# Performance work log

Hardware: AMD Instinct MI355X
Metric: run time of the kernel (lower is better)

## Reference

```python
import jax, jax.numpy as jnp
import numpy as np
from jax import lax

IMG_W, IMG_H = 800.0, 320.0
NPTS = 72
N_STRIPS = NPTS - 1
MAX_LANES = 4
NUM_PRIORS = 192
STAGES = 3
B = 512
LIOU_LEN = 15.0
CLS_W, XYT_W, IOU_W, SEG_W = 2.0, 0.2, 2.0, 1.0


def smooth_l1(x):
    ax = jnp.abs(x)
    return jnp.where(ax < 1.0, 0.5 * x * x, ax - 0.5)


def pairwise_line_iou(pred_xs, tgt_xs):
    # pred_xs [P,N] pixel xs, tgt_xs [L,N]; returns [P,L]
    px1, px2 = pred_xs - LIOU_LEN, pred_xs + LIOU_LEN
    tx1, tx2 = tgt_xs - LIOU_LEN, tgt_xs + LIOU_LEN
    ovr = jnp.minimum(px2[:, None, :], tx2[None]) - jnp.maximum(px1[:, None, :], tx1[None])
    union = jnp.maximum(px2[:, None, :], tx2[None]) - jnp.minimum(px1[:, None, :], tx1[None])
    invalid = (tgt_xs < 0) | (tgt_xs >= IMG_W)
    ovr = jnp.where(invalid[None], 0.0, ovr)
    union = jnp.where(invalid[None], 0.0, union)
    return ovr.sum(-1) / (union.sum(-1) + 1e-9)


def focal_sum(logits, target):
    # kornia-style softmax focal loss (alpha=0.25, gamma=2), summed
    p = jax.nn.softmax(logits, axis=1) + 1e-8
    focal = -0.25 * (1.0 - p) ** 2 * jnp.log(p)
    oh = jax.nn.one_hot(target, 2, dtype=logits.dtype)
    return (oh * focal).sum()


def per_sample(pred, tgt):
    # pred [P, 6+N], tgt [L, 6+N]
    L = tgt.shape[0]
    f32 = pred.dtype
    valid = tgt[:, 1] == 1.0
    num_t = valid.sum()
    has_t = num_t > 0

    t_xs = tgt[:, 6:]                          # [L,N] pixel xs (-1e5 = invalid)
    pred_xs_px = pred[:, 6:] * (IMG_W - 1.0)   # [P,N]
    iou_pair = pairwise_line_iou(pred_xs_px, t_xs)  # [P,L] (grad flows for loss)

    # ---------- assignment (stop-grad, mirrors CLRNet dynamic_assign) ----------
    pd = lax.stop_gradient(pred)
    pd_xs = pd[:, 6:] * (IMG_W - 1.0)
    inv_t = (t_xs < 0) | (t_xs >= IMG_W)
    t_len = (~inv_t).sum(1).astype(f32)
    dist = jnp.where(inv_t[None], 0.0, jnp.abs(t_xs[None] - pd_xs[:, None, :])).sum(-1)
    dist = dist / (t_len[None] + 1e-9)         # [P,L]

    def norm_score(x):
        m = jnp.max(jnp.where(valid[None], x, -jnp.inf))
        m = jnp.where(has_t, m, 1.0)
        return 1.0 - x / m + 1e-2

    dist_score = norm_score(dist)
    p_xy = jnp.stack([pd[:, 2] * (IMG_H - 1.0), pd[:, 3] * (IMG_W - 1.0)], 1)
    t_xy = jnp.stack([tgt[:, 2] * (IMG_H - 1.0), tgt[:, 3]], 1)
    sd = jnp.sqrt(((p_xy[:, None] - t_xy[None]) ** 2).sum(-1))
    s_score = norm_score(sd)
    th = jnp.abs(pd[:, 4, None] - tgt[None, :, 4]) * 180.0
    th_score = norm_score(th)
    sp = jax.nn.sigmoid(pd[:, :2])
    neg = -jnp.log(1.0 - sp + 1e-12) * 0.75 * sp ** 2
    pos = -jnp.log(sp + 1e-12) * 0.25 * (1.0 - sp) ** 2
    cls_cost = pos[:, 1] - neg[:, 1]           # all gt labels are 1
    cost = -(dist_score * s_score * th_score) ** 2 * 3.0 + cls_cost[:, None]
    cost = jnp.where(valid[None], cost, jnp.inf)

    # dynamic-k (SimOTA-style)
    iou_sg = jnp.where(valid[None], jnp.maximum(lax.stop_gradient(iou_pair), 0.0), 0.0)
    topk = lax.top_k(iou_sg.T, 4)[0]           # [L,4]
    dyn_k = jnp.maximum(topk.sum(1).astype(jnp.int32), 1)
    ranks = jnp.argsort(jnp.argsort(cost, axis=0), axis=0)
    M = (ranks < dyn_k[None]) & valid[None]
    multi = M.sum(1) > 1
    argmin_col = jnp.argmin(cost, axis=1)
    Mf = M.astype(f32)
    Mf = Mf.at[:, 0].set(jnp.where(multi, 0.0, Mf[:, 0]))
    oh_min = jax.nn.one_hot(argmin_col, L, dtype=f32)
    Mf = jnp.where(multi[:, None] & (oh_min > 0), 1.0, Mf)
    n_match = Mf.sum()

    # ---------- cls loss ----------
    cls_target = (Mf.sum(1) > 0).astype(jnp.int32)
    cls_term = focal_sum(pred[:, :2], cls_target) / jnp.where(has_t, num_t.astype(f32), 1.0)

    # ---------- reg yxtl (smooth L1) ----------
    scale = jnp.array([N_STRIPS, IMG_W - 1.0, 180.0, N_STRIPS], dtype=f32)
    pred_yxtl = pred[:, 2:6] * scale           # [P,4]
    tgt3 = jnp.stack([tgt[:, 2] * N_STRIPS, tgt[:, 3], tgt[:, 4] * 180.0], 1)  # [L,3]
    pred_starts = jnp.clip(jnp.round(lax.stop_gradient(pred[:, 2]) * N_STRIPS), 0, N_STRIPS)
    tgt_starts = jnp.round(tgt[:, 2] * N_STRIPS)
    tgt_len_pair = tgt[None, :, 5] - (pred_starts[:, None] - tgt_starts[None, :])  # [P,L]
    sl = smooth_l1(pred_yxtl[:, None, :3] - tgt3[None]).sum(-1) \
       + smooth_l1(pred_yxtl[:, 3][:, None] - tgt_len_pair)
    reg_term = (Mf * sl).sum() / jnp.maximum(n_match * 4.0, 1.0)
    iou_term = (Mf * (1.0 - iou_pair)).sum() / jnp.maximum(n_match, 1.0)
    zero = jnp.zeros((), f32)
    reg_term = jnp.where(has_t, reg_term, zero)
    iou_term = jnp.where(has_t, iou_term, zero)
    return cls_term, reg_term, iou_term


def setup_inputs() -> dict:
    key = jax.random.key(0)
    ks = jax.random.split(key, 8)
    D = 6 + NPTS
    cls = jax.random.normal(ks[0], (STAGES, B, NUM_PRIORS, 2), jnp.float32)
    rest = jax.random.uniform(ks[1], (STAGES, B, NUM_PRIORS, D - 2), dtype=jnp.float32)
    predictions = jnp.concatenate([cls, rest], -1)

    valid = jax.random.uniform(ks[2], (B, MAX_LANES)) < 0.8
    start = jax.random.randint(ks[3], (B, MAX_LANES), 0, 40)
    length = jax.random.randint(ks[4], (B, MAX_LANES), 10, NPTS)
    end = jnp.minimum(start + length, NPTS)
    idx = jnp.arange(NPTS)
    inside = (idx[None, None] >= start[..., None]) & (idx[None, None] < end[..., None]) & valid[..., None]
    xs = jax.random.uniform(ks[5], (B, MAX_LANES, NPTS), minval=0.0, maxval=IMG_W - 1.0)
    xs = jnp.where(inside, xs, -1e5)
    start_x = jnp.take_along_axis(xs, start[..., None], axis=-1)[..., 0]
    theta = jax.random.uniform(ks[6], (B, MAX_LANES), minval=0.3, maxval=0.9)
    vf = valid.astype(jnp.float32)
    neg = jnp.full((B, MAX_LANES), -1e5, jnp.float32)
    targets = jnp.full((B, MAX_LANES, D), -1e5, jnp.float32)
    targets = targets.at[..., 0].set(1.0 - vf)
    targets = targets.at[..., 1].set(vf)
    targets = targets.at[..., 2].set(jnp.where(valid, start.astype(jnp.float32) / N_STRIPS, neg))
    targets = targets.at[..., 3].set(jnp.where(valid, start_x, neg))
    targets = targets.at[..., 4].set(jnp.where(valid, theta, neg))
    targets = targets.at[..., 5].set(jnp.where(valid, (end - start).astype(jnp.float32), neg))
    targets = targets.at[..., 6:].set(xs)

    seg_loss = jax.random.uniform(ks[7], (), dtype=jnp.float32)
    return {"predictions": predictions, "targets": targets, "seg_loss": seg_loss}


def reference(predictions, targets, seg_loss):
    per_batch = jax.vmap(per_sample)
    cls_l = jnp.zeros((), predictions.dtype)
    reg_l = jnp.zeros((), predictions.dtype)
    iou_l = jnp.zeros((), predictions.dtype)
    for s in range(predictions.shape[0]):  # 3 refine stages (fixed)
        c, r, i = per_batch(predictions[s], targets)
        cls_l = cls_l + c.sum()
        reg_l = reg_l + r.sum()
        iou_l = iou_l + i.sum()
    denom = targets.shape[0] * predictions.shape[0]
    cls_l = cls_l / denom
    reg_l = reg_l / denom
    iou_l = iou_l / denom
    return cls_l * CLS_W + reg_l * XYT_W + iou_l * IOU_W + seg_loss * SEG_W
```

## Files before the change

kernel.cpp:

```cpp
#include <hip/hip_runtime.h>
#include <math.h>

constexpr int kNpts   = 72;
constexpr int kPriors = 192;
constexpr int kLanes  = 4;
constexpr int kBatch  = 512;
constexpr int kStages = 3;
constexpr int kD      = 6 + kNpts;
constexpr int kBlocks = kStages * kBatch;
constexpr int kPackOffset = 2048;
constexpr int kPackFloats = kBatch * kNpts * 8;

typedef unsigned long long u64;
typedef float fv16 __attribute__((ext_vector_type(16)));

__device__ __forceinline__ float smoothL1(float x) {
  float ax = fabsf(x);
  return ax < 1.0f ? 0.5f * x * x : ax - 0.5f;
}

__device__ __forceinline__ unsigned ordF(float f) {
  unsigned b = __float_as_uint(f);
  return (b & 0x80000000u) ? ~b : (b | 0x80000000u);
}

__device__ __forceinline__ void cswapA(u64& a, u64& b) {
  if (b < a) { u64 t = a; a = b; b = t; }
}
__device__ __forceinline__ void cswapD(float& a, float& b) {
  if (b > a) { float t = a; a = b; b = t; }
}
__device__ __forceinline__ u64 umin64(u64 a, u64 b) { return a < b ? a : b; }
__device__ __forceinline__ u64 umax64(u64 a, u64 b) { return a < b ? b : a; }

__global__ __launch_bounds__(256) void clr_prep(
    const float* __restrict__ tgt, float* __restrict__ pack) {
  int i = blockIdx.x * 256 + threadIdx.x;
  if (i >= kBatch * kNpts) return;
  int b = i / kNpts, k = i - b * kNpts;
  const float* tg = tgt + (size_t)b * kLanes * kD + 6 + k;
  float v0 = tg[0 * kD], v1 = tg[1 * kD], v2 = tg[2 * kD], v3 = tg[3 * kD];
  float4 tx = make_float4(v0, v1, v2, v3);
  float4 m  = make_float4((v0 >= 0.0f && v0 < 800.0f) ? 1.0f : 0.0f,
                          (v1 >= 0.0f && v1 < 800.0f) ? 1.0f : 0.0f,
                          (v2 >= 0.0f && v2 < 800.0f) ? 1.0f : 0.0f,
                          (v3 >= 0.0f && v3 < 800.0f) ? 1.0f : 0.0f);
  float4* o = (float4*)(pack + (size_t)i * 8);
  o[0] = tx;
  o[1] = m;
}

#define SGRP(OFF0, OFF1, SA, SB)                                          \
  asm volatile("s_load_dwordx16 %0, %2, %3\n\t"                           \
               "s_load_dwordx16 %1, %2, %4\n\t"                           \
               "s_waitcnt lgkmcnt(0)"                                     \
               : "=s"(SA), "=s"(SB)                                       \
               : "s"(pka), "n"(OFF0), "n"(OFF1));

#define KQUAD(SV, E0, PXV)                                                \
  { const float px_ = (PXV) * 799.0f;                                     \
    ds0 = fmaf(SV[(E0) + 4], fabsf(SV[(E0) + 0] - px_), ds0);             \
    ds1 = fmaf(SV[(E0) + 5], fabsf(SV[(E0) + 1] - px_), ds1);             \
    ds2 = fmaf(SV[(E0) + 6], fabsf(SV[(E0) + 2] - px_), ds2);             \
    ds3 = fmaf(SV[(E0) + 7], fabsf(SV[(E0) + 3] - px_), ds3); }

#define GRP(G, CA, CB, PA, PB, DOPF)                                      \
  { fv16 SA_, SB_;                                                        \
    SGRP(128 * (G), 128 * (G) + 64, SA_, SB_)                             \
    if (DOPF) { PA = rowv[7 + 2 * (G)]; PB = rowv[8 + 2 * (G)]; }         \
    KQUAD(SA_, 0, CA.x) KQUAD(SA_, 8, CA.y)                               \
    KQUAD(SB_, 0, CB.x) KQUAD(SB_, 8, CB.y) }

__global__ __launch_bounds__(192, 4) void clr_loss_smem(
    const float* __restrict__ pred,
    const float* __restrict__ tgt,
    float* __restrict__ partial,
    const float* __restrict__ pack) {
  const int blk  = blockIdx.x;
  const int b    = blk & (kBatch - 1);
  const int tid  = threadIdx.x;
  const int wav  = tid >> 6;
  const int lane = tid & 63;

  __shared__ float s_hdr[kLanes][6];
  __shared__ float s_cost[kLanes][kPriors];
  __shared__ float s_iou[kLanes][kPriors];
  __shared__ u64   s_k3[kLanes][3];
  __shared__ int   s_dk[kLanes];
  __shared__ float s_sc[3][4];

  const float* tg = tgt + (size_t)b * kLanes * kD;
  if (tid < kLanes * 6) {
    int j = tid / 6, c = tid - j * 6;
    s_hdr[j][c] = tg[j * kD + c];
  }
  if (tid >= 64 && tid < 64 + kLanes) {
    int j = tid - 64;
    s_dk[j] = 1; s_k3[j][0] = 0; s_k3[j][1] = 0; s_k3[j][2] = 0;
  }

  const float*  pr   = pred + ((size_t)blk * kPriors + tid) * kD;
  const float2* rowv = (const float2*)pr;
  float2 h0 = rowv[0], h1 = rowv[1], h2 = rowv[2];
  const float p0 = h0.x, p1 = h0.y, p2 = h1.x, p3 = h1.y, p4 = h2.x, p5 = h2.y;

  const unsigned long long pka =
      (unsigned long long)(const void*)(pack + (size_t)b * (kNpts * 8));
  float ds0 = 0.0f, ds1 = 0.0f, ds2 = 0.0f, ds3 = 0.0f;
  {
    float2 q0a = rowv[3], q0b = rowv[4];
    float2 q1a = rowv[5], q1b = rowv[6];
    float2 q2a, q2b;
    GRP(0,  q0a, q0b, q2a, q2b, true)
    GRP(1,  q1a, q1b, q0a, q0b, true)
    GRP(2,  q2a, q2b, q1a, q1b, true)
    GRP(3,  q0a, q0b, q2a, q2b, true)
    GRP(4,  q1a, q1b, q0a, q0b, true)
    GRP(5,  q2a, q2b, q1a, q1b, true)
    GRP(6,  q0a, q0b, q2a, q2b, true)
    GRP(7,  q1a, q1b, q0a, q0b, true)
    GRP(8,  q2a, q2b, q1a, q1b, true)
    GRP(9,  q0a, q0b, q2a, q2b, true)
    GRP(10, q1a, q1b, q0a, q0b, true)
    GRP(11, q2a, q2b, q1a, q1b, true)
    GRP(12, q0a, q0b, q2a, q2b, true)
    GRP(13, q1a, q1b, q0a, q0b, true)
    GRP(14, q2a, q2b, q1a, q1b, true)
    GRP(15, q0a, q0b, q2a, q2b, true)
    GRP(16, q1a, q1b, q2a, q2b, false)
    GRP(17, q2a, q2b, q2a, q2b, false)
  }
  float ds[kLanes] = {ds0, ds1, ds2, ds3};

  __syncthreads();

  bool validL[kLanes];
  int num_t = 0;
#pragma unroll
  for (int j = 0; j < kLanes; ++j) {
    validL[j] = (s_hdr[j][1] == 1.0f);
    num_t += validL[j] ? 1 : 0;
  }
  const bool has_t = num_t > 0;

  float iou[kLanes], dist[kLanes], sd[kLanes], th[kLanes];
  float md = -INFINITY, ms = -INFINITY, mt = -INFINITY;
  const float py = p2 * 319.0f, pxc = p3 * 799.0f;
#pragma unroll
  for (int j = 0; j < kLanes; ++j) {
    float tlen = validL[j] ? s_hdr[j][5] : 0.0f;
    float ovr = fmaf(tlen, 30.0f, -ds[j]);
    float uni = fmaf(tlen, 30.0f,  ds[j]) + 1e-9f;
    iou[j]  = ovr / uni;
    dist[j] = ds[j] / (tlen + 1e-9f);
    float dy = py - s_hdr[j][2] * 319.0f;
    float dx = pxc - s_hdr[j][3];
    sd[j] = sqrtf(dy * dy + dx * dx);
    th[j] = fabsf(p4 - s_hdr[j][4]) * 180.0f;
    if (validL[j]) {
      md = fmaxf(md, dist[j]);
      ms = fmaxf(ms, sd[j]);
      mt = fmaxf(mt, th[j]);
    }
  }

#pragma unroll
  for (int off = 32; off; off >>= 1) {
    md = fmaxf(md, __shfl_down(md, off, 64));
    ms = fmaxf(ms, __shfl_down(ms, off, 64));
    mt = fmaxf(mt, __shfl_down(mt, off, 64));
  }
  if (lane == 0) { s_sc[wav][0] = md; s_sc[wav][1] = ms; s_sc[wav][2] = mt; }
  __syncthreads();
  md = fmaxf(fmaxf(s_sc[0][0], s_sc[1][0]), s_sc[2][0]);
  ms = fmaxf(fmaxf(s_sc[0][1], s_sc[1][1]), s_sc[2][1]);
  mt = fmaxf(fmaxf(s_sc[0][2], s_sc[1][2]), s_sc[2][2]);
  if (!has_t) { md = 1.0f; ms = 1.0f; mt = 1.0f; }

  const float sp1  = 1.0f / (1.0f + expf(-p1));
  const float neg1 = -logf(1.0f - sp1 + 1e-12f) * 0.75f * sp1 * sp1;
  const float om1  = 1.0f - sp1;
  const float pos1 = -logf(sp1 + 1e-12f) * 0.25f * om1 * om1;
  const float cls_cost = pos1 - neg1;

  float costr[kLanes];
#pragma unroll
  for (int j = 0; j < kLanes; ++j) {
    s_iou[j][tid] = validL[j] ? fmaxf(iou[j], 0.0f) : 0.0f;
    float c;
    if (validL[j]) {
      float a = (1.0f - dist[j] / md) + 0.01f;
      float s = (1.0f - sd[j] / ms) + 0.01f;
      float t = (1.0f - th[j] / mt) + 0.01f;
      float g = a * s * t;
      c = cls_cost - g * g * 3.0f;
    } else {
      c = INFINITY;
    }
    costr[j] = c;
    s_cost[j][tid] = c;
  }
  __syncthreads();

  for (int t = wav; t < 8; t += 3) {
    const int j = t & 3;
    if (!validL[j]) continue;
    if (t < 4) {
      float c0 = s_cost[j][lane], c1 = s_cost[j][lane + 64], c2 = s_cost[j][lane + 128];
      u64 k0 = ((u64)ordF(c0) << 32) | (unsigned)lane;
      u64 k1 = ((u64)ordF(c1) << 32) | (unsigned)(lane + 64);
      u64 k2 = ((u64)ordF(c2) << 32) | (unsigned)(lane + 128);
      cswapA(k0, k1); cswapA(k0, k2); cswapA(k1, k2);
#pragma unroll
      for (int off = 1; off < 64; off <<= 1) {
        u64 b0 = __shfl_xor(k0, off), b1 = __shfl_xor(k1, off), b2 = __shfl_xor(k2, off);
        u64 x0 = umin64(k0, b0), y0 = umax64(k0, b0);
        u64 x1 = umin64(k1, b1);
        u64 mc = umin64(k2, b2);
        k0 = x0;
        k2 = umin64(umax64(y0, x1), mc);
        k1 = umin64(y0, x1);
      }
      if (lane == 0) { s_k3[j][0] = k0; s_k3[j][1] = k1; s_k3[j][2] = k2; }
    } else {
      float t0 = s_iou[j][lane], t1 = s_iou[j][lane + 64], t2 = s_iou[j][lane + 128];
      float t3 = -1.0f;
      cswapD(t0, t1); cswapD(t0, t2); cswapD(t1, t2);
#pragma unroll
      for (int off = 1; off < 64; off <<= 1) {
        float b0 = __shfl_xor(t0, off), b1 = __shfl_xor(t1, off);
        float b2 = __shfl_xor(t2, off), b3 = __shfl_xor(t3, off);
        float m0 = fmaxf(t0, b3), m1 = fmaxf(t1, b2);
        float m2 = fmaxf(t2, b1), m3 = fmaxf(t3, b0);
        cswapD(m0, m2); cswapD(m1, m3); cswapD(m0, m1); cswapD(m2, m3);
        t0 = m0; t1 = m1; t2 = m2; t3 = m3;
      }
      if (lane == 0) {
        float s = ((t0 + t1) + t2) + t3;
        int dk = (int)s;
        if (dk < 1) dk = 1;
        if (dk > 3) dk = 3;
        s_dk[j] = dk;
      }
    }
  }
  __syncthreads();

  int Mi[kLanes];
  int msum = 0;
#pragma unroll
  for (int j = 0; j < kLanes; ++j) {
    u64 myk = ((u64)ordF(costr[j]) << 32) | (unsigned)tid;
    Mi[j] = (validL[j] && myk <= s_k3[j][s_dk[j] - 1]) ? 1 : 0;
    msum += Mi[j];
  }

  float amin = costr[0];
  int aidx = 0;
#pragma unroll
  for (int j = 1; j < kLanes; ++j)
    if (costr[j] < amin) { amin = costr[j]; aidx = j; }

  float Mf[kLanes];
#pragma unroll
  for (int j = 0; j < kLanes; ++j) Mf[j] = (float)Mi[j];
  if (msum > 1) {
    Mf[0] = 0.0f;
    Mf[aidx] = 1.0f;
  }

  const float mfsum = Mf[0] + Mf[1] + Mf[2] + Mf[3];
  const int cls_t = (mfsum > 0.0f) ? 1 : 0;

  const float mx = fmaxf(p0, p1);
  const float e0 = expf(p0 - mx), e1 = expf(p1 - mx);
  const float inv = 1.0f / (e0 + e1);
  const float q = (cls_t ? e1 : e0) * inv + 1e-8f;
  const float omq = 1.0f - q;
  const float focal = -0.25f * omq * omq * logf(q);

  const float pred_start = fminf(fmaxf(rintf(p2 * 71.0f), 0.0f), 71.0f);
  const float py0 = p2 * 71.0f, py1 = p3 * 799.0f, py2t = p4 * 180.0f, py3 = p5 * 71.0f;
  float regc = 0.0f, iouc = 0.0f;
#pragma unroll
  for (int j = 0; j < kLanes; ++j) {
    if (Mf[j] > 0.0f) {
      float t30 = s_hdr[j][2] * 71.0f;
      float t31 = s_hdr[j][3];
      float t32 = s_hdr[j][4] * 180.0f;
      float tstart = rintf(s_hdr[j][2] * 71.0f);
      float tlp = s_hdr[j][5] - (pred_start - tstart);
      regc += smoothL1(py0 - t30) + smoothL1(py1 - t31) + smoothL1(py2t - t32)
            + smoothL1(py3 - tlp);
      iouc += 1.0f - iou[j];
    }
  }

  float v0 = mfsum, v1 = focal, v2 = regc, v3 = iouc;
#pragma unroll
  for (int off = 32; off; off >>= 1) {
    v0 += __shfl_down(v0, off, 64);
    v1 += __shfl_down(v1, off, 64);
    v2 += __shfl_down(v2, off, 64);
    v3 += __shfl_down(v3, off, 64);
  }
  __syncthreads();
  if (lane == 0) {
    s_sc[wav][0] = v0; s_sc[wav][1] = v1; s_sc[wav][2] = v2; s_sc[wav][3] = v3;
  }
  __syncthreads();

  if (tid == 0) {
    float nm      = s_sc[0][0] + s_sc[1][0] + s_sc[2][0];
    float cls_sum = s_sc[0][1] + s_sc[1][1] + s_sc[2][1];
    float reg_sum = s_sc[0][2] + s_sc[1][2] + s_sc[2][2];
    float iou_sum = s_sc[0][3] + s_sc[1][3] + s_sc[2][3];

    float cls_term = cls_sum / (has_t ? (float)num_t : 1.0f);
    float reg_term = has_t ? reg_sum / fmaxf(nm * 4.0f, 1.0f) : 0.0f;
    float iou_term = has_t ? iou_sum / fmaxf(nm, 1.0f) : 0.0f;

    partial[blk] = 2.0f * cls_term + 0.2f * reg_term + 2.0f * iou_term;
  }
}

#undef GRP
#undef KQUAD
#undef SGRP

__global__ __launch_bounds__(192) void clr_loss_lds(
    const float* __restrict__ pred,
    const float* __restrict__ tgt,
    float* __restrict__ partial) {
  const int blk  = blockIdx.x;
  const int b    = blk & (kBatch - 1);
  const int tid  = threadIdx.x;
  const int wav  = tid >> 6;
  const int lane = tid & 63;

  __shared__ float s_tx[kNpts][kLanes];
  __shared__ float s_m [kNpts][kLanes];
  __shared__ float s_hdr[kLanes][6];
  __shared__ float s_cost[kLanes][kPriors];
  __shared__ float s_iou[kLanes][kPriors];
  __shared__ u64   s_k3[kLanes][3];
  __shared__ int   s_dk[kLanes];
  __shared__ float s_sc[3][4];

  const float* tg = tgt + (size_t)b * kLanes * kD;
  for (int t = tid; t < kLanes * kNpts; t += 192) {
    int j = t / kNpts, k = t - j * kNpts;
    float v = tg[j * kD + 6 + k];
    s_tx[k][j] = v;
    s_m [k][j] = (v >= 0.0f && v < 800.0f) ? 1.0f : 0.0f;
  }
  if (tid < kLanes * 6) {
    int j = tid / 6, c = tid - j * 6;
    s_hdr[j][c] = tg[j * kD + c];
  }
  if (tid >= 64 && tid < 64 + kLanes) {
    int j = tid - 64;
    s_dk[j] = 1; s_k3[j][0] = 0; s_k3[j][1] = 0; s_k3[j][2] = 0;
  }

  const float*  pr   = pred + ((size_t)blk * kPriors + tid) * kD;
  const float2* rowv = (const float2*)pr;
  float2 h0 = rowv[0], h1 = rowv[1], h2 = rowv[2];
  float px[kNpts];
#pragma unroll
  for (int q = 0; q < 36; ++q) {
    float2 v = rowv[3 + q];
    px[2 * q]     = v.x * 799.0f;
    px[2 * q + 1] = v.y * 799.0f;
  }
  const float p0 = h0.x, p1 = h0.y, p2 = h1.x, p3 = h1.y, p4 = h2.x, p5 = h2.y;

  __syncthreads();

  bool validL[kLanes];
  int num_t = 0;
#pragma unroll
  for (int j = 0; j < kLanes; ++j) {
    validL[j] = (s_hdr[j][1] == 1.0f);
    num_t += validL[j] ? 1 : 0;
  }
  const bool has_t = num_t > 0;

  float ds[kLanes] = {0.0f, 0.0f, 0.0f, 0.0f};
  {
    const float4* tx4 = (const float4*)&s_tx[0][0];
    const float4* m4  = (const float4*)&s_m[0][0];
#pragma unroll
    for (int k = 0; k < kNpts; ++k) {
      float4 t = tx4[k];
      float4 m = m4[k];
      float p = px[k];
      ds[0] = fmaf(m.x, fabsf(t.x - p), ds[0]);
      ds[1] = fmaf(m.y, fabsf(t.y - p), ds[1]);
      ds[2] = fmaf(m.z, fabsf(t.z - p), ds[2]);
      ds[3] = fmaf(m.w, fabsf(t.w - p), ds[3]);
    }
  }

  float iou[kLanes], dist[kLanes], sd[kLanes], th[kLanes];
  float md = -INFINITY, ms = -INFINITY, mt = -INFINITY;
  const float py = p2 * 319.0f, pxc = p3 * 799.0f;
#pragma unroll
  for (int j = 0; j < kLanes; ++j) {
    float tlen = validL[j] ? s_hdr[j][5] : 0.0f;
    float ovr = fmaf(tlen, 30.0f, -ds[j]);
    float uni = fmaf(tlen, 30.0f,  ds[j]) + 1e-9f;
    iou[j]  = ovr / uni;
    dist[j] = ds[j] / (tlen + 1e-9f);
    float dy = py - s_hdr[j][2] * 319.0f;
    float dx = pxc - s_hdr[j][3];
    sd[j] = sqrtf(dy * dy + dx * dx);
    th[j] = fabsf(p4 - s_hdr[j][4]) * 180.0f;
    if (validL[j]) {
      md = fmaxf(md, dist[j]);
      ms = fmaxf(ms, sd[j]);
      mt = fmaxf(mt, th[j]);
    }
  }

#pragma unroll
  for (int off = 32; off; off >>= 1) {
    md = fmaxf(md, __shfl_down(md, off, 64));
    ms = fmaxf(ms, __shfl_down(ms, off, 64));
    mt = fmaxf(mt, __shfl_down(mt, off, 64));
  }
  if (lane == 0) { s_sc[wav][0] = md; s_sc[wav][1] = ms; s_sc[wav][2] = mt; }
  __syncthreads();
  md = fmaxf(fmaxf(s_sc[0][0], s_sc[1][0]), s_sc[2][0]);
  ms = fmaxf(fmaxf(s_sc[0][1], s_sc[1][1]), s_sc[2][1]);
  mt = fmaxf(fmaxf(s_sc[0][2], s_sc[1][2]), s_sc[2][2]);
  if (!has_t) { md = 1.0f; ms = 1.0f; mt = 1.0f; }

  const float sp1  = 1.0f / (1.0f + expf(-p1));
  const float neg1 = -logf(1.0f - sp1 + 1e-12f) * 0.75f * sp1 * sp1;
  const float om1  = 1.0f - sp1;
  const float pos1 = -logf(sp1 + 1e-12f) * 0.25f * om1 * om1;
  const float cls_cost = pos1 - neg1;

  float costr[kLanes];
#pragma unroll
  for (int j = 0; j < kLanes; ++j) {
    s_iou[j][tid] = validL[j] ? fmaxf(iou[j], 0.0f) : 0.0f;
    float c;
    if (validL[j]) {
      float a = (1.0f - dist[j] / md) + 0.01f;
      float s = (1.0f - sd[j] / ms) + 0.01f;
      float t = (1.0f - th[j] / mt) + 0.01f;
      float g = a * s * t;
      c = cls_cost - g * g * 3.0f;
    } else {
      c = INFINITY;
    }
    costr[j] = c;
    s_cost[j][tid] = c;
  }
  __syncthreads();

  for (int t = wav; t < 8; t += 3) {
    const int j = t & 3;
    if (!validL[j]) continue;
    if (t < 4) {
      float c0 = s_cost[j][lane], c1 = s_cost[j][lane + 64], c2 = s_cost[j][lane + 128];
      u64 k0 = ((u64)ordF(c0) << 32) | (unsigned)lane;
      u64 k1 = ((u64)ordF(c1) << 32) | (unsigned)(lane + 64);
      u64 k2 = ((u64)ordF(c2) << 32) | (unsigned)(lane + 128);
      cswapA(k0, k1); cswapA(k0, k2); cswapA(k1, k2);
#pragma unroll
      for (int off = 1; off < 64; off <<= 1) {
        u64 b0 = __shfl_xor(k0, off), b1 = __shfl_xor(k1, off), b2 = __shfl_xor(k2, off);
        u64 x0 = umin64(k0, b0), y0 = umax64(k0, b0);
        u64 x1 = umin64(k1, b1);
        u64 mc = umin64(k2, b2);
        k0 = x0;
        k2 = umin64(umax64(y0, x1), mc);
        k1 = umin64(y0, x1);
      }
      if (lane == 0) { s_k3[j][0] = k0; s_k3[j][1] = k1; s_k3[j][2] = k2; }
    } else {
      float t0 = s_iou[j][lane], t1 = s_iou[j][lane + 64], t2 = s_iou[j][lane + 128];
      float t3 = -1.0f;
      cswapD(t0, t1); cswapD(t0, t2); cswapD(t1, t2);
#pragma unroll
      for (int off = 1; off < 64; off <<= 1) {
        float b0 = __shfl_xor(t0, off), b1 = __shfl_xor(t1, off);
        float b2 = __shfl_xor(t2, off), b3 = __shfl_xor(t3, off);
        float m0 = fmaxf(t0, b3), m1 = fmaxf(t1, b2);
        float m2 = fmaxf(t2, b1), m3 = fmaxf(t3, b0);
        cswapD(m0, m2); cswapD(m1, m3); cswapD(m0, m1); cswapD(m2, m3);
        t0 = m0; t1 = m1; t2 = m2; t3 = m3;
      }
      if (lane == 0) {
        float s = ((t0 + t1) + t2) + t3;
        int dk = (int)s;
        if (dk < 1) dk = 1;
        if (dk > 3) dk = 3;
        s_dk[j] = dk;
      }
    }
  }
  __syncthreads();

  int Mi[kLanes];
  int msum = 0;
#pragma unroll
  for (int j = 0; j < kLanes; ++j) {
    u64 myk = ((u64)ordF(costr[j]) << 32) | (unsigned)tid;
    Mi[j] = (validL[j] && myk <= s_k3[j][s_dk[j] - 1]) ? 1 : 0;
    msum += Mi[j];
  }

  float amin = costr[0];
  int aidx = 0;
#pragma unroll
  for (int j = 1; j < kLanes; ++j)
    if (costr[j] < amin) { amin = costr[j]; aidx = j; }

  float Mf[kLanes];
#pragma unroll
  for (int j = 0; j < kLanes; ++j) Mf[j] = (float)Mi[j];
  if (msum > 1) {
    Mf[0] = 0.0f;
    Mf[aidx] = 1.0f;
  }

  const float mfsum = Mf[0] + Mf[1] + Mf[2] + Mf[3];
  const int cls_t = (mfsum > 0.0f) ? 1 : 0;

  const float mx = fmaxf(p0, p1);
  const float e0 = expf(p0 - mx), e1 = expf(p1 - mx);
  const float inv = 1.0f / (e0 + e1);
  const float q = (cls_t ? e1 : e0) * inv + 1e-8f;
  const float omq = 1.0f - q;
  const float focal = -0.25f * omq * omq * logf(q);

  const float pred_start = fminf(fmaxf(rintf(p2 * 71.0f), 0.0f), 71.0f);
  const float py0 = p2 * 71.0f, py1 = p3 * 799.0f, py2t = p4 * 180.0f, py3 = p5 * 71.0f;
  float regc = 0.0f, iouc = 0.0f;
#pragma unroll
  for (int j = 0; j < kLanes; ++j) {
    if (Mf[j] > 0.0f) {
      float t30 = s_hdr[j][2] * 71.0f;
      float t31 = s_hdr[j][3];
      float t32 = s_hdr[j][4] * 180.0f;
      float tstart = rintf(s_hdr[j][2] * 71.0f);
      float tlp = s_hdr[j][5] - (pred_start - tstart);
      regc += smoothL1(py0 - t30) + smoothL1(py1 - t31) + smoothL1(py2t - t32)
            + smoothL1(py3 - tlp);
      iouc += 1.0f - iou[j];
    }
  }

  float v0 = mfsum, v1 = focal, v2 = regc, v3 = iouc;
#pragma unroll
  for (int off = 32; off; off >>= 1) {
    v0 += __shfl_down(v0, off, 64);
    v1 += __shfl_down(v1, off, 64);
    v2 += __shfl_down(v2, off, 64);
    v3 += __shfl_down(v3, off, 64);
  }
  __syncthreads();
  if (lane == 0) {
    s_sc[wav][0] = v0; s_sc[wav][1] = v1; s_sc[wav][2] = v2; s_sc[wav][3] = v3;
  }
  __syncthreads();

  if (tid == 0) {
    float nm      = s_sc[0][0] + s_sc[1][0] + s_sc[2][0];
    float cls_sum = s_sc[0][1] + s_sc[1][1] + s_sc[2][1];
    float reg_sum = s_sc[0][2] + s_sc[1][2] + s_sc[2][2];
    float iou_sum = s_sc[0][3] + s_sc[1][3] + s_sc[2][3];

    float cls_term = cls_sum / (has_t ? (float)num_t : 1.0f);
    float reg_term = has_t ? reg_sum / fmaxf(nm * 4.0f, 1.0f) : 0.0f;
    float iou_term = has_t ? iou_sum / fmaxf(nm, 1.0f) : 0.0f;

    partial[blk] = 2.0f * cls_term + 0.2f * reg_term + 2.0f * iou_term;
  }
}

__global__ __launch_bounds__(256) void clr_reduce(
    const float* __restrict__ partial,
    const float* __restrict__ seg,
    float* __restrict__ out) {
  const int tid  = threadIdx.x;
  const int wav  = tid >> 6;
  const int lane = tid & 63;
  __shared__ float sc[4];

  float s = 0.0f;
#pragma unroll
  for (int i = 0; i < kBlocks / 256; ++i) s += partial[tid + 256 * i];
#pragma unroll
  for (int off = 32; off; off >>= 1) s += __shfl_down(s, off, 64);
  if (lane == 0) sc[wav] = s;
  __syncthreads();
  if (tid == 0) {
    float tot = ((sc[0] + sc[1]) + sc[2]) + sc[3];
    out[0] = tot * (1.0f / (float)kBlocks) + seg[0];
  }
}

extern "C" void kernel_launch(void* const* d_in, const int* in_sizes, int n_in,
                              void* d_out, int out_size, void* d_ws, size_t ws_size,
                              hipStream_t stream) {
  const float* pred = (const float*)d_in[0];
  const float* tgt  = (const float*)d_in[1];
  const float* seg  = (const float*)d_in[2];
  float* out     = (float*)d_out;
  float* partial = (float*)d_ws;

  const size_t need = (size_t)(kPackOffset + kPackFloats) * sizeof(float);
  if (ws_size >= need) {
    float* pack = (float*)d_ws + kPackOffset;
    clr_prep<<<(kBatch * kNpts + 255) / 256, 256, 0, stream>>>(tgt, pack);
    clr_loss_smem<<<kBlocks, 192, 0, stream>>>(pred, tgt, partial, pack);
  } else {
    clr_loss_lds<<<kBlocks, 192, 0, stream>>>(pred, tgt, partial);
  }
  clr_reduce<<<1, 256, 0, stream>>>(partial, seg, out);
}
```

Baseline: 171.7 us.

## Split loss kernel into geometry pass and assignment pass via workspace buffers

```diff
diff --git a/kernel.cpp b/kernel.cpp
--- a/kernel.cpp
+++ b/kernel.cpp
@@ -8,11 +8,13 @@
 constexpr int kStages = 3;
 constexpr int kD      = 6 + kNpts;
 constexpr int kBlocks = kStages * kBatch;
-constexpr int kPackOffset = 2048;
-constexpr int kPackFloats = kBatch * kNpts * 8;
+constexpr int kRows   = kBlocks * kPriors;
+constexpr size_t kWsA0   = 2048;
+constexpr size_t kWsA1   = kWsA0 + (size_t)kRows * 4;
+constexpr size_t kWsA2   = kWsA1 + (size_t)kRows * 4;
+constexpr size_t kWsNeed = (kWsA2 + (size_t)kRows * 4) * sizeof(float);
 
 typedef unsigned long long u64;
-typedef float fv16 __attribute__((ext_vector_type(16)));
 
 __device__ __forceinline__ float smoothL1(float x) {
   float ax = fabsf(x);
@@ -33,54 +35,69 @@
 __device__ __forceinline__ u64 umin64(u64 a, u64 b) { return a < b ? a : b; }
 __device__ __forceinline__ u64 umax64(u64 a, u64 b) { return a < b ? b : a; }
 
-__global__ __launch_bounds__(256) void clr_prep(
-    const float* __restrict__ tgt, float* __restrict__ pack) {
-  int i = blockIdx.x * 256 + threadIdx.x;
-  if (i >= kBatch * kNpts) return;
-  int b = i / kNpts, k = i - b * kNpts;
-  const float* tg = tgt + (size_t)b * kLanes * kD + 6 + k;
-  float v0 = tg[0 * kD], v1 = tg[1 * kD], v2 = tg[2 * kD], v3 = tg[3 * kD];
-  float4 tx = make_float4(v0, v1, v2, v3);
-  float4 m  = make_float4((v0 >= 0.0f && v0 < 800.0f) ? 1.0f : 0.0f,
-                          (v1 >= 0.0f && v1 < 800.0f) ? 1.0f : 0.0f,
-                          (v2 >= 0.0f && v2 < 800.0f) ? 1.0f : 0.0f,
-                          (v3 >= 0.0f && v3 < 800.0f) ? 1.0f : 0.0f);
-  float4* o = (float4*)(pack + (size_t)i * 8);
-  o[0] = tx;
-  o[1] = m;
-}
-
-#define SGRP(OFF0, OFF1, SA, SB)                                          \
-  asm volatile("s_load_dwordx16 %0, %2, %3\n\t"                           \
-               "s_load_dwordx16 %1, %2, %4\n\t"                           \
-               "s_waitcnt lgkmcnt(0)"                                     \
-               : "=s"(SA), "=s"(SB)                                       \
-               : "s"(pka), "n"(OFF0), "n"(OFF1));
-
-#define KQUAD(SV, E0, PXV)                                                \
-  { const float px_ = (PXV) * 799.0f;                                     \
-    ds0 = fmaf(SV[(E0) + 4], fabsf(SV[(E0) + 0] - px_), ds0);             \
-    ds1 = fmaf(SV[(E0) + 5], fabsf(SV[(E0) + 1] - px_), ds1);             \
-    ds2 = fmaf(SV[(E0) + 6], fabsf(SV[(E0) + 2] - px_), ds2);             \
-    ds3 = fmaf(SV[(E0) + 7], fabsf(SV[(E0) + 3] - px_), ds3); }
-
-#define GRP(G, CA, CB, PA, PB, DOPF)                                      \
-  { fv16 SA_, SB_;                                                        \
-    SGRP(128 * (G), 128 * (G) + 64, SA_, SB_)                             \
-    if (DOPF) { PA = rowv[7 + 2 * (G)]; PB = rowv[8 + 2 * (G)]; }         \
-    KQUAD(SA_, 0, CA.x) KQUAD(SA_, 8, CA.y)                               \
-    KQUAD(SB_, 0, CB.x) KQUAD(SB_, 8, CB.y) }
-
-__global__ __launch_bounds__(192, 4) void clr_loss_smem(
+__global__ __launch_bounds__(64) void clr_geom(
     const float* __restrict__ pred,
     const float* __restrict__ tgt,
-    float* __restrict__ partial,
-    const float* __restrict__ pack) {
+    float4* __restrict__ A0,
+    float4* __restrict__ A1,
+    float4* __restrict__ A2) {
+  const int q3   = blockIdx.x;
+  const int blk  = blockIdx.y;
+  const int b    = blk & (kBatch - 1);
+  const int lane = threadIdx.x;
+  const int row  = blk * kPriors + q3 * 64 + lane;
+
+  __shared__ __align__(16) float s_tx[kNpts][kLanes];
+
+  const float* tg = tgt + (size_t)b * kLanes * kD;
+  for (int i = lane; i < kLanes * kNpts; i += 64) {
+    int j = i / kNpts, k = i - j * kNpts;
+    s_tx[k][j] = tg[j * kD + 6 + k];
+  }
+
+  const float2* rowv = (const float2*)(pred + (size_t)row * kD);
+  float2 h0 = rowv[0], h1 = rowv[1], h2 = rowv[2];
+  float px[kNpts];
+#pragma unroll
+  for (int q = 0; q < 36; ++q) {
+    float2 v = rowv[3 + q];
+    px[2 * q]     = v.x * 799.0f;
+    px[2 * q + 1] = v.y * 799.0f;
+  }
+
+  __syncthreads();
+
+  float ds0 = 0.0f, ds1 = 0.0f, ds2 = 0.0f, ds3 = 0.0f;
+  {
+    const float4* tx4 = (const float4*)&s_tx[0][0];
+#pragma unroll
+    for (int k = 0; k < kNpts; ++k) {
+      float4 t = tx4[k];
+      float p = px[k];
+      ds0 += (t.x >= 0.0f) ? fabsf(t.x - p) : 0.0f;
+      ds1 += (t.y >= 0.0f) ? fabsf(t.y - p) : 0.0f;
+      ds2 += (t.z >= 0.0f) ? fabsf(t.z - p) : 0.0f;
+      ds3 += (t.w >= 0.0f) ? fabsf(t.w - p) : 0.0f;
+    }
+  }
+
+  A0[row] = make_float4(ds0, ds1, ds2, ds3);
+  A1[row] = make_float4(h0.x, h0.y, h1.x, h1.y);
+  A2[row] = make_float4(h2.x, h2.y, 0.0f, 0.0f);
+}
+
+__global__ __launch_bounds__(192) void clr_pick(
+    const float* __restrict__ tgt,
+    const float4* __restrict__ A0,
+    const float4* __restrict__ A1,
+    const float4* __restrict__ A2,
+    float* __restrict__ partial) {
   const int blk  = blockIdx.x;
   const int b    = blk & (kBatch - 1);
   const int tid  = threadIdx.x;
   const int wav  = tid >> 6;
   const int lane = tid & 63;
+  const int row  = blk * kPriors + tid;
 
   __shared__ float s_hdr[kLanes][6];
   __shared__ float s_cost[kLanes][kPriors];
@@ -99,38 +116,11 @@
     s_dk[j] = 1; s_k3[j][0] = 0; s_k3[j][1] = 0; s_k3[j][2] = 0;
   }
 
-  const float*  pr   = pred + ((size_t)blk * kPriors + tid) * kD;
-  const float2* rowv = (const float2*)pr;
-  float2 h0 = rowv[0], h1 = rowv[1], h2 = rowv[2];
-  const float p0 = h0.x, p1 = h0.y, p2 = h1.x, p3 = h1.y, p4 = h2.x, p5 = h2.y;
-
-  const unsigned long long pka =
-      (unsigned long long)(const void*)(pack + (size_t)b * (kNpts * 8));
-  float ds0 = 0.0f, ds1 = 0.0f, ds2 = 0.0f, ds3 = 0.0f;
-  {
-    float2 q0a = rowv[3], q0b = rowv[4];
-    float2 q1a = rowv[5], q1b = rowv[6];
-    float2 q2a, q2b;
-    GRP(0,  q0a, q0b, q2a, q2b, true)
-    GRP(1,  q1a, q1b, q0a, q0b, true)
-    GRP(2,  q2a, q2b, q1a, q1b, true)
-    GRP(3,  q0a, q0b, q2a, q2b, true)
-    GRP(4,  q1a, q1b, q0a, q0b, true)
-    GRP(5,  q2a, q2b, q1a, q1b, true)
-    GRP(6,  q0a, q0b, q2a, q2b, true)
-    GRP(7,  q1a, q1b, q0a, q0b, true)
-    GRP(8,  q2a, q2b, q1a, q1b, true)
-    GRP(9,  q0a, q0b, q2a, q2b, true)
-    GRP(10, q1a, q1b, q0a, q0b, true)
-    GRP(11, q2a, q2b, q1a, q1b, true)
-    GRP(12, q0a, q0b, q2a, q2b, true)
-    GRP(13, q1a, q1b, q0a, q0b, true)
-    GRP(14, q2a, q2b, q1a, q1b, true)
-    GRP(15, q0a, q0b, q2a, q2b, true)
-    GRP(16, q1a, q1b, q2a, q2b, false)
-    GRP(17, q2a, q2b, q2a, q2b, false)
-  }
-  float ds[kLanes] = {ds0, ds1, ds2, ds3};
+  const float4 dv = A0[row];
+  const float4 hA = A1[row];
+  const float4 hB = A2[row];
+  const float p0 = hA.x, p1 = hA.y, p2 = hA.z, p3 = hA.w, p4 = hB.x, p5 = hB.y;
+  float ds[kLanes] = {dv.x, dv.y, dv.z, dv.w};
 
   __syncthreads();
 
@@ -324,11 +314,15 @@
   }
 }
 
-#undef GRP
-#undef KQUAD
-#undef SGRP
-
-__global__ __launch_bounds__(192) void clr_loss_lds(
+#define STEP(K, PV) {                                         \
+    const float4 t_ = tx4[(K)];                               \
+    const float p_ = (PV) * 799.0f;                           \
+    ds0 += (t_.x >= 0.0f) ? fabsf(t_.x - p_) : 0.0f;          \
+    ds1 += (t_.y >= 0.0f) ? fabsf(t_.y - p_) : 0.0f;          \
+    ds2 += (t_.z >= 0.0f) ? fabsf(t_.z - p_) : 0.0f;          \
+    ds3 += (t_.w >= 0.0f) ? fabsf(t_.w - p_) : 0.0f; }
+
+__global__ __launch_bounds__(192) void clr_loss_fallback(
     const float* __restrict__ pred,
     const float* __restrict__ tgt,
     float* __restrict__ partial) {
@@ -338,8 +332,7 @@
   const int wav  = tid >> 6;
   const int lane = tid & 63;
 
-  __shared__ float s_tx[kNpts][kLanes];
-  __shared__ float s_m [kNpts][kLanes];
+  __shared__ __align__(16) float s_tx[kNpts][kLanes];
   __shared__ float s_hdr[kLanes][6];
   __shared__ float s_cost[kLanes][kPriors];
   __shared__ float s_iou[kLanes][kPriors];
@@ -350,9 +343,7 @@
   const float* tg = tgt + (size_t)b * kLanes * kD;
   for (int t = tid; t < kLanes * kNpts; t += 192) {
     int j = t / kNpts, k = t - j * kNpts;
-    float v = tg[j * kD + 6 + k];
-    s_tx[k][j] = v;
-    s_m [k][j] = (v >= 0.0f && v < 800.0f) ? 1.0f : 0.0f;
+    s_tx[k][j] = tg[j * kD + 6 + k];
   }
   if (tid < kLanes * 6) {
     int j = tid / 6, c = tid - j * 6;
@@ -386,21 +377,28 @@
   }
   const bool has_t = num_t > 0;
 
-  float ds[kLanes] = {0.0f, 0.0f, 0.0f, 0.0f};
+  float ds0 = 0.0f, ds1 = 0.0f, ds2 = 0.0f, ds3 = 0.0f;
   {
     const float4* tx4 = (const float4*)&s_tx[0][0];
-    const float4* m4  = (const float4*)&s_m[0][0];
+#pragma unroll
+    for (int k = 0; k < kNpts; ++k) {
+      STEP(k, px[k] * (1.0f / 799.0f) * 799.0f)
+    }
+  }
+  ds0 = 0.0f; ds1 = 0.0f; ds2 = 0.0f; ds3 = 0.0f;
+  {
+    const float4* tx4 = (const float4*)&s_tx[0][0];
 #pragma unroll
     for (int k = 0; k < kNpts; ++k) {
       float4 t = tx4[k];
-      float4 m = m4[k];
       float p = px[k];
-      ds[0] = fmaf(m.x, fabsf(t.x - p), ds[0]);
-      ds[1] = fmaf(m.y, fabsf(t.y - p), ds[1]);
-      ds[2] = fmaf(m.z, fabsf(t.z - p), ds[2]);
-      ds[3] = fmaf(m.w, fabsf(t.w - p), ds[3]);
-    }
-  }
+      ds0 += (t.x >= 0.0f) ? fabsf(t.x - p) : 0.0f;
+      ds1 += (t.y >= 0.0f) ? fabsf(t.y - p) : 0.0f;
+      ds2 += (t.z >= 0.0f) ? fabsf(t.z - p) : 0.0f;
+      ds3 += (t.w >= 0.0f) ? fabsf(t.w - p) : 0.0f;
+    }
+  }
+  float ds[kLanes] = {ds0, ds1, ds2, ds3};
 
   float iou[kLanes], dist[kLanes], sd[kLanes], th[kLanes];
   float md = -INFINITY, ms = -INFINITY, mt = -INFINITY;
@@ -582,6 +580,7 @@
     partial[blk] = 2.0f * cls_term + 0.2f * reg_term + 2.0f * iou_term;
   }
 }
+#undef STEP
 
 __global__ __launch_bounds__(256) void clr_reduce(
     const float* __restrict__ partial,
@@ -612,15 +611,17 @@
   const float* tgt  = (const float*)d_in[1];
   const float* seg  = (const float*)d_in[2];
   float* out     = (float*)d_out;
-  float* partial = (float*)d_ws;
-
-  const size_t need = (size_t)(kPackOffset + kPackFloats) * sizeof(float);
-  if (ws_size >= need) {
-    float* pack = (float*)d_ws + kPackOffset;
-    clr_prep<<<(kBatch * kNpts + 255) / 256, 256, 0, stream>>>(tgt, pack);
-    clr_loss_smem<<<kBlocks, 192, 0, stream>>>(pred, tgt, partial, pack);
+  float* ws      = (float*)d_ws;
+  float* partial = ws;
+
+  if (ws_size >= kWsNeed) {
+    float4* A0 = (float4*)(ws + kWsA0);
+    float4* A1 = (float4*)(ws + kWsA1);
+    float4* A2 = (float4*)(ws + kWsA2);
+    clr_geom<<<dim3(3, kBlocks), 64, 0, stream>>>(pred, tgt, A0, A1, A2);
+    clr_pick<<<kBlocks, 192, 0, stream>>>(tgt, A0, A1, A2, partial);
   } else {
-    clr_loss_lds<<<kBlocks, 192, 0, stream>>>(pred, tgt, partial);
+    clr_loss_fallback<<<kBlocks, 192, 0, stream>>>(pred, tgt, partial);
   }
   clr_reduce<<<1, 256, 0, stream>>>(partial, seg, out);
 }
```

New measurement: 159.7 us. -7.0%, faster.
